# Performance work log

Measured on AMD Instinct MI355X. Metric: run time of the kernel, lower is better.

## Reference

```python
import jax, jax.numpy as jnp
import numpy as np

D_HEAD = 128
WINDOW = 512
SCALE = D_HEAD ** -0.5

def setup_inputs() -> dict:
    key = jax.random.key(0)
    kq, kk, kv = jax.random.split(key, 3)
    shape = (4, 16, 2048, D_HEAD)  # [B, H, T, d_head]
    q = jax.random.normal(kq, shape, dtype=jnp.float32)
    k = jax.random.normal(kk, shape, dtype=jnp.float32)
    v = jax.random.normal(kv, shape, dtype=jnp.float32)
    return {"q": q, "k": k, "v": v}

def reference(q, k, v):
    # Sliding-window causal attention (BaseAttention._sliding_window_attention).
    T = q.shape[2]
    scores = jnp.einsum('bhqd,bhkd->bhqk', q, k) * SCALE  # [B,H,T,T]
    i = jnp.arange(T)
    causal = i[None, :] <= i[:, None]                      # j <= i
    in_window = (i[:, None] - i[None, :]) < WINDOW         # i - j < window
    mask = causal & in_window
    scores = jnp.where(mask, scores, -jnp.inf)
    attn = jax.nn.softmax(scores.astype(jnp.float32), axis=-1).astype(v.dtype)
    return jnp.einsum('bhqk,bhkd->bhqd', attn, v)
```

## Files before the change

### kernel.cpp

```cpp
#include <hip/hip_runtime.h>

#define T_SEQ   2048
#define DH      128
#define WINDOW  512
#define BM      128
#define BN      64
#define NT      32
#define TILE_US 16384
#define HALF_US 8192
#define SCALE_LOG2E 0.12751744250f

typedef unsigned short ushort_t;
typedef __attribute__((ext_vector_type(8))) unsigned short ushort8;
typedef __attribute__((ext_vector_type(4))) unsigned short ushort4v;
typedef __attribute__((ext_vector_type(4))) float float4v;
typedef __attribute__((ext_vector_type(16))) float float16v;
typedef __attribute__((ext_vector_type(8))) __bf16 bf16x8;

union U8 { ushort8 us; bf16x8 bf; unsigned u[4]; };
union FU { float f; unsigned u; };

__device__ __forceinline__ unsigned short f2bf(float f) {
  FU x; x.f = f;
  unsigned r = x.u + 0x7FFFu + ((x.u >> 16) & 1u);
  return (unsigned short)(r >> 16);
}

__device__ __forceinline__ void async16(const ushort_t* g, ushort_t* l) {
  __builtin_amdgcn_global_load_lds(
      (const __attribute__((address_space(1))) unsigned int*)g,
      (__attribute__((address_space(3))) unsigned int*)l, 16, 0, 0);
}

__device__ __forceinline__ void stage_half(const ushort_t* __restrict__ src,
                                           ushort_t* __restrict__ dst,
                                           const int tid) {
#pragma unroll
  for (int rd = 0; rd < 4; ++rd) {
    const int off = (rd * 256 + tid) * 8;
    async16(src + off, dst + off);
  }
}

#define WAITV(N) asm volatile("s_waitcnt vmcnt(" #N ")" ::: "memory")
#define MEMFENCE asm volatile("" ::: "memory")

__global__ __launch_bounds__(256)
void pack_kv(const float* __restrict__ kg, const float* __restrict__ vg,
             ushort_t* __restrict__ ws)
{
  __shared__ __align__(16) ushort_t sb[TILE_US];
  const int tile = blockIdx.x;
  const int tid  = threadIdx.x;
  const size_t src = (size_t)tile * (BN * DH);
  const float* kb = kg + src;
  const float* vb = vg + src;

#pragma unroll
  for (int rep = 0; rep < 4; ++rep) {
    const int b   = rep * 256 + tid;
    const int key = b >> 4;
    const int c8  = b & 15;
    const float* s = kb + key * DH + c8 * 8;
    float4v a = *(const float4v*)s;
    float4v c = *(const float4v*)(s + 4);
    U8 h;
    h.us[0]=f2bf(a[0]); h.us[1]=f2bf(a[1]); h.us[2]=f2bf(a[2]); h.us[3]=f2bf(a[3]);
    h.us[4]=f2bf(c[0]); h.us[5]=f2bf(c[1]); h.us[6]=f2bf(c[2]); h.us[7]=f2bf(c[3]);
    *(ushort8*)(sb + key * DH + ((c8 ^ (key & 7)) << 3)) = h.us;
  }

  {
    const int cb  = tid >> 3;
    const int rb0 = tid & 7;
#pragma unroll
    for (int it = 0; it < 2; ++it) {
      const int rb = rb0 + it * 8;
      const float* s = vb + (size_t)(rb * 4) * DH + cb * 4;
      float4v r0 = *(const float4v*)(s);
      float4v r1 = *(const float4v*)(s + DH);
      float4v r2 = *(const float4v*)(s + 2 * DH);
      float4v r3 = *(const float4v*)(s + 3 * DH);
      const int B    = (rb & 1) | ((rb >> 2) << 1);
      const int off4 = ((rb >> 1) & 1) << 2;
#pragma unroll
      for (int c = 0; c < 4; ++c) {
        const int d = cb * 4 + c;
        ushort4v h;
        h[0]=f2bf(r0[c]); h[1]=f2bf(r1[c]); h[2]=f2bf(r2[c]); h[3]=f2bf(r3[c]);
        *(ushort4v*)(sb + 8192 + d * BN + ((B ^ (d & 7)) << 3) + off4) = h;
      }
    }
  }
  __syncthreads();

  ushort_t* wt = ws + (size_t)tile * TILE_US;
#pragma unroll
  for (int rep = 0; rep < 8; ++rep) {
    const int off = (rep * 256 + tid) * 8;
    *(ushort8*)(wt + off) = *(const ushort8*)(sb + off);
  }
}

__global__ __launch_bounds__(256, 3)
void swa_fwd(const float* __restrict__ qg, const ushort_t* __restrict__ ws,
             float* __restrict__ og)
{
  __shared__ __align__(16) ushort_t lds[3 * HALF_US];

  const int qt   = (gridDim.x - 1) - blockIdx.x;
  const int bh   = blockIdx.y;
  const int tid  = threadIdx.x;
  const int wv   = tid >> 6;
  const int lane = tid & 63;
  const int l32  = lane & 31;
  const int half = lane >> 5;
  const int l7   = l32 & 7;

  const size_t base = (size_t)bh * (T_SEQ * DH);
  const float* qb = qg + base;
  float*       ob = og + base;
  const ushort_t* wsb = ws + (size_t)bh * NT * TILE_US;

  const int i0w = qt * BM + wv * 32;
  const int iq  = i0w + l32;

  const int lo  = qt * BM - (WINDOW - 1);
  const int kt0 = (lo > 0) ? (lo >> 6) : 0;
  const int kt1 = 2 * qt + 1;

  int sa = 0, sb = HALF_US, sc = 2 * HALF_US;

  {
    const ushort_t* wt0 = wsb + (size_t)kt0 * TILE_US;
    stage_half(wt0,           lds + sa, tid);
    stage_half(wt0 + HALF_US, lds + sb, tid);
    if (kt0 < kt1)
      stage_half(wt0 + TILE_US, lds + sc, tid);
  }

  bf16x8 qf[8];
  {
    const float* qrow = qb + (size_t)iq * DH + half * 8;
#pragma unroll
    for (int ks = 0; ks < 8; ++ks) {
      float4v a = *(const float4v*)(qrow + ks * 16);
      float4v b = *(const float4v*)(qrow + ks * 16 + 4);
      U8 u;
      u.us[0]=f2bf(a[0]*SCALE_LOG2E); u.us[1]=f2bf(a[1]*SCALE_LOG2E);
      u.us[2]=f2bf(a[2]*SCALE_LOG2E); u.us[3]=f2bf(a[3]*SCALE_LOG2E);
      u.us[4]=f2bf(b[0]*SCALE_LOG2E); u.us[5]=f2bf(b[1]*SCALE_LOG2E);
      u.us[6]=f2bf(b[2]*SCALE_LOG2E); u.us[7]=f2bf(b[3]*SCALE_LOG2E);
      qf[ks] = u.bf;
    }
  }

  float16v O[4];
#pragma unroll
  for (int dc = 0; dc < 4; ++dc) O[dc] = (float16v)(0.0f);
  float m = -1e30f, l = 0.f;

  if (kt0 < kt1) { WAITV(8); } else { WAITV(4); }
  __builtin_amdgcn_s_barrier();
  MEMFENCE;

  for (int kt = kt0; kt <= kt1; ++kt) {
    const int j0 = kt * BN;
    const bool active = (j0 <= i0w + 31) && (i0w - j0 - 63 < WINDOW);

    float16v sv[2];
    if (active) {
      __builtin_amdgcn_s_setprio(1);
#pragma unroll
      for (int c = 0; c < 2; ++c) {
        float16v acc = (float16v)(0.0f);
        const ushort_t* krow = lds + sa + (c * 32 + l32) * DH;
#pragma unroll
        for (int ks = 0; ks < 8; ++ks) {
          U8 a; a.us = *(const ushort8*)(krow + (((2 * ks + half) ^ l7) << 3));
          acc = __builtin_amdgcn_mfma_f32_32x32x16_bf16(a.bf, qf[ks], acc, 0, 0, 0);
        }
        sv[c] = acc;
      }
      __builtin_amdgcn_s_setprio(0);
    }

    MEMFENCE;
    __builtin_amdgcn_s_barrier();
    MEMFENCE;
    if (kt < kt1)
      stage_half(wsb + (size_t)(kt + 1) * TILE_US + HALF_US, lds + sa, tid);

    if (active) {
      const bool full = (j0 + 63 <= i0w) && ((i0w + 31) - j0 < WINDOW);
      if (!full) {
#pragma unroll
        for (int c = 0; c < 2; ++c) {
#pragma unroll
          for (int r = 0; r < 16; ++r) {
            const int j = j0 + c * 32 + (r & 3) + 8 * (r >> 2) + 4 * half;
            const bool ok = (j <= iq) && ((iq - j) < WINDOW);
            sv[c][r] = ok ? sv[c][r] : -1e30f;
          }
        }
      }

      float mt = sv[0][0];
#pragma unroll
      for (int r = 1; r < 16; ++r) mt = fmaxf(mt, sv[0][r]);
#pragma unroll
      for (int r = 0; r < 16; ++r) mt = fmaxf(mt, sv[1][r]);
      mt = fmaxf(mt, __shfl_xor(mt, 32));
      const float mn = fmaxf(m, mt);
      const float alpha = __builtin_amdgcn_exp2f(m - mn);
      m = mn;

      float ps = 0.f;
      unsigned pk[2][8];
#pragma unroll
      for (int c = 0; c < 2; ++c) {
#pragma unroll
        for (int rg = 0; rg < 8; ++rg) {
          FU p0, p1;
          p0.f = __builtin_amdgcn_exp2f(sv[c][2 * rg]     - m);
          p1.f = __builtin_amdgcn_exp2f(sv[c][2 * rg + 1] - m);
          p0.u &= 0xFFFF0000u; p1.u &= 0xFFFF0000u;
          ps += p0.f + p1.f;
          pk[c][rg] = (p0.u >> 16) | p1.u;
        }
      }
      l = l * alpha + ps;
#pragma unroll
      for (int dc = 0; dc < 4; ++dc)
#pragma unroll
        for (int r = 0; r < 16; ++r) O[dc][r] *= alpha;

      if (kt < kt1) { WAITV(8); } else { WAITV(0); }
      __builtin_amdgcn_s_barrier();
      MEMFENCE;

      __builtin_amdgcn_s_setprio(1);
#pragma unroll
      for (int s = 0; s < 4; ++s) {
        const int c = s >> 1, o = (s & 1) * 4;
        U8 b;
        b.u[0] = pk[c][o]; b.u[1] = pk[c][o + 1];
        b.u[2] = pk[c][o + 2]; b.u[3] = pk[c][o + 3];
        const int blk = ((2 * s + half) ^ l7) << 3;
#pragma unroll
        for (int dc = 0; dc < 4; ++dc) {
          U8 a; a.us = *(const ushort8*)(lds + sb + (dc * 32 + l32) * BN + blk);
          O[dc] = __builtin_amdgcn_mfma_f32_32x32x16_bf16(a.bf, b.bf, O[dc], 0, 0, 0);
        }
      }
      __builtin_amdgcn_s_setprio(0);
    } else {
      if (kt < kt1) { WAITV(8); } else { WAITV(0); }
      __builtin_amdgcn_s_barrier();
      MEMFENCE;
    }

    if (kt < kt1) {
      MEMFENCE;
      __builtin_amdgcn_s_barrier();
      MEMFENCE;
      if (kt + 2 <= kt1) {
        stage_half(wsb + (size_t)(kt + 2) * TILE_US, lds + sb, tid);
        WAITV(8);
      } else {
        WAITV(4);
      }
      __builtin_amdgcn_s_barrier();
      MEMFENCE;
    }

    const int t = sc; sc = sb; sb = sa; sa = t;
  }

  l += __shfl_xor(l, 32);
  const float linv = 1.0f / l;
  float* orow = ob + (size_t)iq * DH;
#pragma unroll
  for (int dc = 0; dc < 4; ++dc) {
#pragma unroll
    for (int g = 0; g < 4; ++g) {
      float4v o4;
      o4[0] = O[dc][g * 4 + 0] * linv; o4[1] = O[dc][g * 4 + 1] * linv;
      o4[2] = O[dc][g * 4 + 2] * linv; o4[3] = O[dc][g * 4 + 3] * linv;
      *(float4v*)(orow + dc * 32 + g * 8 + half * 4) = o4;
    }
  }
}

extern "C" void kernel_launch(void* const* d_in, const int* in_sizes, int n_in,
                              void* d_out, int out_size, void* d_ws, size_t ws_size,
                              hipStream_t stream) {
  const float* q = (const float*)d_in[0];
  const float* k = (const float*)d_in[1];
  const float* v = (const float*)d_in[2];
  float* o = (float*)d_out;
  const int bh_count = in_sizes[0] / (T_SEQ * DH);
  ushort_t* ws = (ushort_t*)d_ws;

  pack_kv<<<dim3(bh_count * NT), 256, 0, stream>>>(k, v, ws);
  swa_fwd<<<dim3(T_SEQ / BM, bh_count), 256, 0, stream>>>(q, ws, o);
}
```

Measured before the change: 308.0 us.

## Restructure K/V staging barriers and drop wave priority hints

Reworks the triple-buffered K/V LDS pipeline synchronisation. It cuts the per-tile barriers from four to two by moving the vmcnt waits in front of the remaining barriers, always prefetches the third half-tile, and removes the s_setprio raises around the MFMA blocks. The goal is less barrier stall inside the inner loop. The tradeoff is that V data is now awaited earlier, before the softmax rather than just before the PV matmul, which can expose more load latency. The unconditional prefetch may also read one tile past the last needed one.

```diff
diff --git a/kernel.cpp b/kernel.cpp
--- a/kernel.cpp
+++ b/kernel.cpp
@@ -44,6 +44,7 @@
 
 #define WAITV(N) asm volatile("s_waitcnt vmcnt(" #N ")" ::: "memory")
 #define MEMFENCE asm volatile("" ::: "memory")
+#define BAR() do { MEMFENCE; __builtin_amdgcn_s_barrier(); MEMFENCE; } while (0)
 
 __global__ __launch_bounds__(256)
 void pack_kv(const float* __restrict__ kg, const float* __restrict__ vg,
@@ -135,8 +136,7 @@
     const ushort_t* wt0 = wsb + (size_t)kt0 * TILE_US;
     stage_half(wt0,           lds + sa, tid);
     stage_half(wt0 + HALF_US, lds + sb, tid);
-    if (kt0 < kt1)
-      stage_half(wt0 + TILE_US, lds + sc, tid);
+    stage_half(wt0 + TILE_US, lds + sc, tid);
   }
 
   bf16x8 qf[8];
@@ -160,9 +160,8 @@
   for (int dc = 0; dc < 4; ++dc) O[dc] = (float16v)(0.0f);
   float m = -1e30f, l = 0.f;
 
-  if (kt0 < kt1) { WAITV(8); } else { WAITV(4); }
-  __builtin_amdgcn_s_barrier();
-  MEMFENCE;
+  WAITV(8);
+  BAR();
 
   for (int kt = kt0; kt <= kt1; ++kt) {
     const int j0 = kt * BN;
@@ -170,7 +169,6 @@
 
     float16v sv[2];
     if (active) {
-      __builtin_amdgcn_s_setprio(1);
 #pragma unroll
       for (int c = 0; c < 2; ++c) {
         float16v acc = (float16v)(0.0f);
@@ -182,12 +180,10 @@
         }
         sv[c] = acc;
       }
-      __builtin_amdgcn_s_setprio(0);
-    }
-
-    MEMFENCE;
-    __builtin_amdgcn_s_barrier();
-    MEMFENCE;
+    }
+
+    if (kt < kt1) { WAITV(4); } else { WAITV(0); }
+    BAR();
     if (kt < kt1)
       stage_half(wsb + (size_t)(kt + 1) * TILE_US + HALF_US, lds + sa, tid);
 
@@ -235,11 +231,6 @@
 #pragma unroll
         for (int r = 0; r < 16; ++r) O[dc][r] *= alpha;
 
-      if (kt < kt1) { WAITV(8); } else { WAITV(0); }
-      __builtin_amdgcn_s_barrier();
-      MEMFENCE;
-
-      __builtin_amdgcn_s_setprio(1);
 #pragma unroll
       for (int s = 0; s < 4; ++s) {
         const int c = s >> 1, o = (s & 1) * 4;
@@ -253,25 +244,13 @@
           O[dc] = __builtin_amdgcn_mfma_f32_32x32x16_bf16(a.bf, b.bf, O[dc], 0, 0, 0);
         }
       }
-      __builtin_amdgcn_s_setprio(0);
-    } else {
-      if (kt < kt1) { WAITV(8); } else { WAITV(0); }
-      __builtin_amdgcn_s_barrier();
-      MEMFENCE;
     }
 
     if (kt < kt1) {
-      MEMFENCE;
-      __builtin_amdgcn_s_barrier();
-      MEMFENCE;
-      if (kt + 2 <= kt1) {
+      WAITV(4);
+      BAR();
+      if (kt + 2 <= kt1)
         stage_half(wsb + (size_t)(kt + 2) * TILE_US, lds + sb, tid);
-        WAITV(8);
-      } else {
-        WAITV(4);
-      }
-      __builtin_amdgcn_s_barrier();
-      MEMFENCE;
     }
 
     const int t = sc; sc = sb; sb = sa; sa = t;
```

New measurement: 306.8 us. No clear change (-0.4%).
